# Kernel optimization log

Hardware: AMD Instinct MI355X
Metric: run time of the kernel (lower is better)

The kernel has to match this reference:

```python
import jax, jax.numpy as jnp
import numpy as np

B, TQ, TV, D = 32, 1024, 1024, 512


def setup_inputs() -> dict:
    key = jax.random.key(0)
    k1, k2, k3, k4 = jax.random.split(key, 4)
    scale = 1.0 / np.sqrt(D)
    return {
        "query": jax.random.normal(k1, (B, TQ, D), dtype=jnp.float32),
        "value": jax.random.normal(k2, (B, TV, D), dtype=jnp.float32),
        "w_weight": jax.random.normal(k3, (D, D), dtype=jnp.float32) * scale,
        "w_bias": jax.random.normal(k4, (D,), dtype=jnp.float32) * scale,
    }


def reference(query, value, w_weight, w_bias):
    # torch Linear: v @ W^T + b  -> keys [B, Tv, D]
    keys = jnp.einsum("bvd,ed->bve", value, w_weight) + w_bias
    # scores [B, Tq, Tv], softmax over Tv (last dim), unscaled as in source
    scores = jnp.einsum("bqd,bvd->bqv", query, keys)
    alignment = jax.nn.softmax(scores, axis=-1)
    context = jnp.einsum("bqv,bvd->bqd", alignment, value)
    context = jnp.concatenate([context, query], axis=-1)  # [B, Tq, 2D]
    alignment_t = jnp.swapaxes(alignment, 1, 2)  # [B, Tv, Tq]
    return context, alignment_t
```

## Files before the change

### kernel.cpp

```cpp
#include <hip/hip_runtime.h>
#include <hip/hip_bf16.h>

#define NB  32
#define NTQ 1024
#define NTV 1024
#define ND  512

typedef float f32x4 __attribute__((ext_vector_type(4)));
typedef float f32x2 __attribute__((ext_vector_type(2)));
typedef __bf16 bf16x8 __attribute__((ext_vector_type(8)));
typedef unsigned short u16x4 __attribute__((ext_vector_type(4)));
typedef unsigned short u16x8 __attribute__((ext_vector_type(8)));
typedef unsigned int u32x2 __attribute__((ext_vector_type(2)));
typedef unsigned int u32x4 __attribute__((ext_vector_type(4)));

static __device__ __forceinline__ unsigned short f2bf(float f) {
  unsigned u = __builtin_bit_cast(unsigned, f);
  u += 0x7fffu + ((u >> 16) & 1u);
  return (unsigned short)(u >> 16);
}
static __device__ __forceinline__ float bf2f(unsigned short h) {
  unsigned u = ((unsigned)h) << 16;
  return __builtin_bit_cast(float, u);
}
static __device__ __forceinline__ unsigned split2(float x) {
  unsigned u = __builtin_bit_cast(unsigned, x);
  unsigned h = u >> 16;
  float hf = __builtin_bit_cast(float, u & 0xffff0000u);
  unsigned l = __builtin_bit_cast(unsigned, x - hf) >> 16;
  return h | (l << 16);
}
static __device__ __forceinline__ f32x4 mfma16(bf16x8 a, bf16x8 b, f32x4 c) {
  return __builtin_amdgcn_mfma_f32_16x16x32_bf16(a, b, c, 0, 0, 0);
}

__global__ __launch_bounds__(256) void k_vt(const float* __restrict__ V,
                                            unsigned short* __restrict__ Vt) {
  int vt = blockIdx.x, dt = blockIdx.y, b = blockIdx.z;
  int t = threadIdx.x;
  __shared__ unsigned short L[64][72];
#pragma unroll
  for (int r = 0; r < 4; ++r) {
    int v = (t >> 4) + r * 16;
    int c4 = (t & 15) * 4;
    f32x4 x = *(const f32x4*)(V + (size_t)(b * NTV + vt * 64 + v) * ND + dt * 64 + c4);
    u16x4 h;
#pragma unroll
    for (int j = 0; j < 4; ++j) h[j] = f2bf(x[j]);
    *(u16x4*)&L[v][c4] = h;
  }
  __syncthreads();
#pragma unroll
  for (int r = 0; r < 4; ++r) {
    int d = (t >> 4) + r * 16;
    int v4 = (t & 15) * 4;
    u16x4 o;
#pragma unroll
    for (int i = 0; i < 4; ++i) o[i] = L[v4 + i][d];
    *(u16x4*)(Vt + (size_t)(b * ND + dt * 64 + d) * NTV + vt * 64 + v4) = o;
  }
}

__global__ __launch_bounds__(256, 2) void k_keys(const float* __restrict__ V,
                                                 const float* __restrict__ W,
                                                 const float* __restrict__ bias,
                                                 unsigned int* __restrict__ kbuf) {
  int bid = blockIdx.x;
  int swz = (bid & 7) * 128 + (bid >> 3);
  int bm = swz >> 2, bn = swz & 3;
  int t = threadIdx.x, lane = t & 63, w = t >> 6;
  int wr = (w >> 1) * 64, wc = (w & 1) * 64;
  __shared__ __align__(16) unsigned char SMEM[73728];
  auto Ah = (unsigned short(*)[72])(SMEM);
  auto Al = (unsigned short(*)[72])(SMEM + 18432);
  auto Bh = (unsigned short(*)[72])(SMEM + 36864);
  auto Bl = (unsigned short(*)[72])(SMEM + 55296);
  f32x4 acc[4][4] = {};
  const int row0 = bm * 128, col0 = bn * 128;
  int srow = t >> 4, c4 = (t & 15) * 4;

  f32x4 vreg[8], wreg[8];
#pragma unroll
  for (int r = 0; r < 8; ++r) {
    vreg[r] = *(const f32x4*)(V + (size_t)(row0 + srow + r * 16) * ND + c4);
    wreg[r] = *(const f32x4*)(W + (size_t)(col0 + srow + r * 16) * ND + c4);
  }
  for (int k0 = 0; k0 < ND; k0 += 64) {
    __syncthreads();
#pragma unroll
    for (int r = 0; r < 8; ++r) {
      int row = srow + r * 16;
      u16x4 h, l;
#pragma unroll
      for (int j = 0; j < 4; ++j) {
        unsigned p = split2(vreg[r][j]);
        h[j] = (unsigned short)(p & 0xffffu); l[j] = (unsigned short)(p >> 16);
      }
      *(u16x4*)&Ah[row][c4] = h; *(u16x4*)&Al[row][c4] = l;
#pragma unroll
      for (int j = 0; j < 4; ++j) {
        unsigned p = split2(wreg[r][j]);
        h[j] = (unsigned short)(p & 0xffffu); l[j] = (unsigned short)(p >> 16);
      }
      *(u16x4*)&Bh[row][c4] = h; *(u16x4*)&Bl[row][c4] = l;
    }
    __syncthreads();
    if (k0 + 64 < ND) {
#pragma unroll
      for (int r = 0; r < 8; ++r) {
        vreg[r] = *(const f32x4*)(V + (size_t)(row0 + srow + r * 16) * ND + k0 + 64 + c4);
        wreg[r] = *(const f32x4*)(W + (size_t)(col0 + srow + r * 16) * ND + k0 + 64 + c4);
      }
    }
#pragma unroll
    for (int kk = 0; kk < 2; ++kk) {
      int kof = kk * 32 + ((lane >> 4) << 3);
      bf16x8 ah[4], al[4], bh[4], bl[4];
#pragma unroll
      for (int i = 0; i < 4; ++i) {
        int ra = wr + i * 16 + (lane & 15);
        ah[i] = *(const bf16x8*)&Ah[ra][kof];
        al[i] = *(const bf16x8*)&Al[ra][kof];
        int rb = wc + i * 16 + (lane & 15);
        bh[i] = *(const bf16x8*)&Bh[rb][kof];
        bl[i] = *(const bf16x8*)&Bl[rb][kof];
      }
#pragma unroll
      for (int i = 0; i < 4; ++i)
#pragma unroll
        for (int j = 0; j < 4; ++j) {
          acc[i][j] = mfma16(ah[i], bh[j], acc[i][j]);
          acc[i][j] = mfma16(ah[i], bl[j], acc[i][j]);
          acc[i][j] = mfma16(al[i], bh[j], acc[i][j]);
        }
    }
  }
  __syncthreads();
  unsigned* CT = (unsigned*)SMEM;
#pragma unroll
  for (int j = 0; j < 4; ++j) {
    int col_l = wc + j * 16 + (lane & 15);
    float bj = bias[col0 + col_l];
#pragma unroll
    for (int i = 0; i < 4; ++i) {
      int rb_l = wr + i * 16 + ((lane >> 4) << 2);
#pragma unroll
      for (int r = 0; r < 4; ++r) CT[(rb_l + r) * 134 + col_l] = split2(acc[i][j][r] + bj);
    }
  }
  __syncthreads();
#pragma unroll
  for (int it = 0; it < 32; ++it) {
    int idx = it * 256 + t;
    int row = idx >> 6, c2 = idx & 63;
    *(u32x2*)(kbuf + (size_t)(row0 + row) * 1024 + col0 + c2 * 2) =
        *(const u32x2*)&CT[row * 134 + c2 * 2];
  }
}

__global__ __launch_bounds__(256, 2) void k_scores(const float* __restrict__ Q,
                                                   const unsigned int* __restrict__ kbuf,
                                                   unsigned short* __restrict__ ebase,
                                                   float2* __restrict__ partials) {
  int bid = blockIdx.x;
  int swz = (bid & 7) * 256 + (bid >> 3);
  int b = swz >> 6, rr2 = swz & 63, vt = rr2 >> 3, qt = rr2 & 7;
  int t = threadIdx.x, lane = t & 63, w = t >> 6, g = lane >> 4, l15 = lane & 15;
  int wr = (w >> 1) * 64, wc = (w & 1) * 64;
  __shared__ __align__(16) unsigned char SMEM[73728];
  auto Ah = (unsigned short(*)[72])(SMEM);
  auto Al = (unsigned short(*)[72])(SMEM + 18432);
  auto Bh = (unsigned short(*)[72])(SMEM + 36864);
  auto Bl = (unsigned short(*)[72])(SMEM + 55296);
  f32x4 acc[4][4] = {};
  const size_t qrow = (size_t)(b * NTQ + qt * 128);
  const size_t krow = (size_t)(b * NTV + vt * 128);
  int srow = t >> 4, c4 = (t & 15) * 4;

  f32x4 qreg[8]; u32x4 kreg[8];
#pragma unroll
  for (int r = 0; r < 8; ++r) {
    qreg[r] = *(const f32x4*)(Q + (qrow + srow + r * 16) * ND + c4);
    kreg[r] = *(const u32x4*)(kbuf + (krow + srow + r * 16) * 1024 + c4);
  }
  for (int k0 = 0; k0 < ND; k0 += 64) {
    __syncthreads();
#pragma unroll
    for (int r = 0; r < 8; ++r) {
      int row = srow + r * 16;
      u16x4 h, l;
#pragma unroll
      for (int j = 0; j < 4; ++j) {
        unsigned p = split2(qreg[r][j]);
        h[j] = (unsigned short)(p & 0xffffu); l[j] = (unsigned short)(p >> 16);
      }
      *(u16x4*)&Ah[row][c4] = h; *(u16x4*)&Al[row][c4] = l;
#pragma unroll
      for (int j = 0; j < 4; ++j) {
        h[j] = (unsigned short)(kreg[r][j] & 0xffffu);
        l[j] = (unsigned short)(kreg[r][j] >> 16);
      }
      *(u16x4*)&Bh[row][c4] = h; *(u16x4*)&Bl[row][c4] = l;
    }
    __syncthreads();
    if (k0 + 64 < ND) {
#pragma unroll
      for (int r = 0; r < 8; ++r) {
        qreg[r] = *(const f32x4*)(Q + (qrow + srow + r * 16) * ND + k0 + 64 + c4);
        kreg[r] = *(const u32x4*)(kbuf + (krow + srow + r * 16) * 1024 + k0 + 64 + c4);
      }
    }
#pragma unroll
    for (int kk = 0; kk < 2; ++kk) {
      int kof = kk * 32 + ((lane >> 4) << 3);
      bf16x8 ah[4], al[4], bh[4], bl[4];
#pragma unroll
      for (int i = 0; i < 4; ++i) {
        int ra = wr + i * 16 + (lane & 15);
        ah[i] = *(const bf16x8*)&Ah[ra][kof];
        al[i] = *(const bf16x8*)&Al[ra][kof];
        int rb = wc + i * 16 + (lane & 15);
        bh[i] = *(const bf16x8*)&Bh[rb][kof];
        bl[i] = *(const bf16x8*)&Bl[rb][kof];
      }
#pragma unroll
      for (int i = 0; i < 4; ++i)
#pragma unroll
        for (int j = 0; j < 4; ++j) {
          acc[i][j] = mfma16(ah[i], bh[j], acc[i][j]);
          acc[i][j] = mfma16(ah[i], bl[j], acc[i][j]);
          acc[i][j] = mfma16(al[i], bh[j], acc[i][j]);
        }
    }
  }
  __syncthreads();
  auto E2 = (unsigned short(*)[136])(SMEM);
  float* Lm = (float*)(SMEM + 36864);
  float* Ls = (float*)(SMEM + 37888);
#pragma unroll
  for (int i = 0; i < 4; ++i)
#pragma unroll
    for (int r = 0; r < 4; ++r) {
      float m = fmaxf(fmaxf(acc[i][0][r], acc[i][1][r]), fmaxf(acc[i][2][r], acc[i][3][r]));
#pragma unroll
      for (int msk = 1; msk < 16; msk <<= 1) m = fmaxf(m, __shfl_xor(m, msk));
      if (l15 == 0) Lm[(wr + i * 16 + g * 4 + r) * 2 + (w & 1)] = m;
    }
  __syncthreads();
#pragma unroll
  for (int i = 0; i < 4; ++i)
#pragma unroll
    for (int r = 0; r < 4; ++r) {
      int ql = wr + i * 16 + g * 4 + r;
      float mf = fmaxf(Lm[ql * 2], Lm[ql * 2 + 1]);
      float s = 0.f;
#pragma unroll
      for (int j = 0; j < 4; ++j) {
        float e = __expf(acc[i][j][r] - mf);
        s += e;
        E2[ql][wc + j * 16 + l15] = f2bf(e);
      }
#pragma unroll
      for (int msk = 1; msk < 16; msk <<= 1) s += __shfl_xor(s, msk);
      if (l15 == 0) Ls[ql * 2 + (w & 1)] = s;
    }
  __syncthreads();
  if (t < 128) {
    float mf = fmaxf(Lm[t * 2], Lm[t * 2 + 1]);
    float lf = Ls[t * 2] + Ls[t * 2 + 1];
    partials[(((size_t)(b * 8 + vt)) << 10) + qt * 128 + t] = make_float2(mf, lf);
  }
#pragma unroll
  for (int it = 0; it < 8; ++it) {
    int idx = it * 256 + t;
    int row = idx >> 4, ch = idx & 15;
    *(u16x8*)(ebase + (size_t)(b * 1024 + qt * 128 + row) * 2048 + 1024 + vt * 128 + ch * 8) =
        *(const u16x8*)&E2[row][ch * 8];
  }
}

__global__ __launch_bounds__(256) void k_combine(const float2* __restrict__ partials,
                                                 float2* __restrict__ stats) {
  int idx = blockIdx.x * 256 + threadIdx.x;
  int b = idx >> 10, q = idx & 1023;
  float2 p[8];
  float M = -3.0e38f;
#pragma unroll
  for (int vt = 0; vt < 8; ++vt) {
    p[vt] = partials[(((size_t)(b * 8 + vt)) << 10) + q];
    M = fmaxf(M, p[vt].x);
  }
  float L = 0.f;
#pragma unroll
  for (int vt = 0; vt < 8; ++vt) L += p[vt].y * __expf(p[vt].x - M);
  stats[idx] = make_float2(M, 1.0f / L);
}

__global__ __launch_bounds__(256, 3) void k_pv(const unsigned short* __restrict__ ebase,
                                               const unsigned short* __restrict__ Vt,
                                               const float2* __restrict__ stats,
                                               const float2* __restrict__ partials,
                                               float* __restrict__ out1) {
  int bid = blockIdx.x;
  int swz = (bid & 7) * 128 + (bid >> 3);
  int b = swz >> 5, qt = (swz >> 2) & 7, dt = swz & 3;
  int t = threadIdx.x, lane = t & 63, w = t >> 6;
  int l15 = lane & 15, g = lane >> 4;
  int wr = (w >> 1) * 64, wc = (w & 1) * 64;
  int q0 = qt * 128, d0 = dt * 128;
  __shared__ __align__(16) unsigned char SMEM[36864];
  auto Ae = (unsigned short(*)[72])(SMEM);
  auto Bv = (unsigned short(*)[72])(SMEM + 18432);
  f32x4 acc[4][4] = {};

  int srow = t >> 3, c8 = (t & 7) * 8;
  float M4[4], iL4[4];
#pragma unroll
  for (int k = 0; k < 4; ++k) {
    float2 st = stats[b * NTQ + q0 + srow + 32 * k];
    M4[k] = st.x; iL4[k] = st.y;
  }
  u16x8 ereg[4], vreg[4];
#pragma unroll
  for (int k = 0; k < 4; ++k) {
    ereg[k] = *(const u16x8*)(ebase + (size_t)(b * 1024 + q0 + srow + 32 * k) * 2048 + 1024 + c8);
    vreg[k] = *(const u16x8*)(Vt + ((size_t)b * ND + d0 + srow + 32 * k) * NTV + c8);
  }
  float sck[4];
  for (int v0 = 0; v0 < NTV; v0 += 64) {
    if ((v0 & 127) == 0) {
      int vt128 = v0 >> 7;
#pragma unroll
      for (int k = 0; k < 4; ++k) {
        float2 p = partials[(((size_t)(b * 8 + vt128)) << 10) + q0 + srow + 32 * k];
        sck[k] = __expf(p.x - M4[k]) * iL4[k];
      }
    }
    __syncthreads();
#pragma unroll
    for (int k = 0; k < 4; ++k) {
      int row = srow + 32 * k;
      u16x8 a;
#pragma unroll
      for (int m = 0; m < 8; ++m) a[m] = f2bf(bf2f(ereg[k][m]) * sck[k]);
      *(u16x8*)&Ae[row][c8] = a;
      *(u16x8*)&Bv[row][c8] = vreg[k];
    }
    if (v0 + 64 < NTV) {
#pragma unroll
      for (int k = 0; k < 4; ++k) {
        ereg[k] = *(const u16x8*)(ebase + (size_t)(b * 1024 + q0 + srow + 32 * k) * 2048 + 1024 + v0 + 64 + c8);
        vreg[k] = *(const u16x8*)(Vt + ((size_t)b * ND + d0 + srow + 32 * k) * NTV + v0 + 64 + c8);
      }
    }
    __syncthreads();
#pragma unroll
    for (int kk = 0; kk < 2; ++kk) {
      int kof = kk * 32 + g * 8;
      bf16x8 af[4], bfr[4];
#pragma unroll
      for (int i = 0; i < 4; ++i) af[i] = *(const bf16x8*)&Ae[wr + i * 16 + l15][kof];
#pragma unroll
      for (int j = 0; j < 4; ++j) bfr[j] = *(const bf16x8*)&Bv[wc + j * 16 + l15][kof];
#pragma unroll
      for (int i = 0; i < 4; ++i)
#pragma unroll
        for (int j = 0; j < 4; ++j) acc[i][j] = mfma16(af[i], bfr[j], acc[i][j]);
    }
  }
  float* CT = (float*)SMEM;
#pragma unroll
  for (int h = 0; h < 2; ++h) {
    __syncthreads();
    if ((w >> 1) == h) {
#pragma unroll
      for (int i = 0; i < 4; ++i)
#pragma unroll
        for (int j = 0; j < 4; ++j) {
          int ql = i * 16 + g * 4;
          int dl = wc + j * 16 + l15;
#pragma unroll
          for (int r = 0; r < 4; ++r) CT[(ql + r) * 132 + dl] = acc[i][j][r];
        }
    }
    __syncthreads();
#pragma unroll
    for (int it = 0; it < 8; ++it) {
      int idx = it * 256 + t;
      int row = idx >> 5, c4 = idx & 31;
      *(f32x4*)(out1 + (size_t)(b * NTQ + q0 + h * 64 + row) * 1024 + d0 + c4 * 4) =
          *(const f32x4*)&CT[row * 132 + c4 * 4];
    }
  }
}

__global__ __launch_bounds__(256) void k_alpha(const unsigned short* ebase,
                                               const float* __restrict__ Q,
                                               const float2* __restrict__ stats,
                                               const float2* __restrict__ partials,
                                               float* __restrict__ out2,
                                               float* out1) {
  int bid = blockIdx.x;
  int swz = (bid & 7) * 64 + (bid >> 3);
  int b = swz >> 4, qc = swz & 15;
  int q0 = qc * 64;
  int t = threadIdx.x;
  __shared__ float T[128][68];
  int row = t >> 4, ch = t & 15;
  float M4[4], iL4[4];
#pragma unroll
  for (int k = 0; k < 4; ++k) {
    float2 st = stats[b * NTQ + q0 + row + 16 * k];
    M4[k] = st.x; iL4[k] = st.y;
  }
  for (int vt = 0; vt < 8; ++vt) {
    __syncthreads();
#pragma unroll
    for (int k = 0; k < 4; ++k) {
      int r = row + 16 * k;
      float2 p = partials[(((size_t)(b * 8 + vt)) << 10) + q0 + r];
      float sc = __expf(p.x - M4[k]) * iL4[k];
      u16x8 ev = *(const u16x8*)(ebase + (size_t)(b * 1024 + q0 + r) * 2048 + 1024 + vt * 128 + ch * 8);
#pragma unroll
      for (int m = 0; m < 8; ++m) {
        int v = ch * 8 + m;
        T[v][r ^ (((v >> 3) & 7) << 3)] = bf2f(ev[m]) * sc;
      }
    }
    __syncthreads();
#pragma unroll
    for (int it = 0; it < 8; ++it) {
      int idx = it * 256 + t;
      int vr = idx >> 4, c4 = idx & 15;
      int cs = (c4 * 4) ^ (((vr >> 3) & 7) << 3);
      *(f32x4*)(out2 + ((size_t)(b * 1024) + vt * 128 + vr) * 1024 + q0 + c4 * 4) =
          *(const f32x4*)&T[vr][cs];
    }
  }
  __syncthreads();
#pragma unroll
  for (int k = 0; k < 32; ++k) {
    int idx = k * 256 + t;
    int r = idx >> 7, c4 = idx & 127;
    *(f32x4*)(out1 + (size_t)(b * 1024 + q0 + r) * 1024 + 512 + c4 * 4) =
        *(const f32x4*)(Q + (size_t)(b * 1024 + q0 + r) * 512 + c4 * 4);
  }
}

extern "C" void kernel_launch(void* const* d_in, const int* in_sizes, int n_in,
                              void* d_out, int out_size, void* d_ws, size_t ws_size,
                              hipStream_t stream) {
  const float* Q    = (const float*)d_in[0];
  const float* V    = (const float*)d_in[1];
  const float* W    = (const float*)d_in[2];
  const float* bias = (const float*)d_in[3];

  float* out1 = (float*)d_out;
  float* out2 = (float*)d_out + (size_t)NB * NTQ * (2 * ND);

  unsigned short* Vt = (unsigned short*)d_ws;
  float2* stats    = (float2*)((char*)d_ws + 33554432);
  float2* partials = (float2*)((char*)d_ws + 33554432 + 262144);

  unsigned int* kbuf = (unsigned int*)out1;
  unsigned short* ebase = (unsigned short*)out1;

  k_vt<<<dim3(16, 8, 32), 256, 0, stream>>>(V, Vt);
  k_keys<<<1024, 256, 0, stream>>>(V, W, bias, kbuf);
  k_scores<<<2048, 256, 0, stream>>>(Q, kbuf, ebase, partials);
  k_combine<<<128, 256, 0, stream>>>(partials, stats);
  k_pv<<<1024, 256, 0, stream>>>(ebase, Vt, stats, partials, out1);
  k_alpha<<<512, 256, 0, stream>>>(ebase, Q, stats, partials, out2, out1);
}
```

Baseline: 341.0 us.

## Halve K-tile and LDS footprint to raise occupancy of GEMM kernels

The keys and scores GEMM kernels now stage 32-wide K tiles instead of 64, halving shared memory per block and the number of prefetch registers. The keys epilogue writes its output through shared memory in two 64-row halves so the staging buffer still fits. Launch bounds are raised to 4 blocks per CU for keys, scores and pv, aiming to hide latency through occupancy. In exchange there are twice as many K iterations and barriers, less unrolled MFMA work per sync, and tighter register caps that risk spills.

```diff
diff --git a/kernel.cpp b/kernel.cpp
--- a/kernel.cpp
+++ b/kernel.cpp
@@ -61,7 +61,7 @@
   }
 }
 
-__global__ __launch_bounds__(256, 2) void k_keys(const float* __restrict__ V,
+__global__ __launch_bounds__(256, 4) void k_keys(const float* __restrict__ V,
                                                  const float* __restrict__ W,
                                                  const float* __restrict__ bias,
                                                  unsigned int* __restrict__ kbuf) {
@@ -69,27 +69,28 @@
   int swz = (bid & 7) * 128 + (bid >> 3);
   int bm = swz >> 2, bn = swz & 3;
   int t = threadIdx.x, lane = t & 63, w = t >> 6;
+  int l15 = lane & 15, g = lane >> 4;
   int wr = (w >> 1) * 64, wc = (w & 1) * 64;
-  __shared__ __align__(16) unsigned char SMEM[73728];
-  auto Ah = (unsigned short(*)[72])(SMEM);
-  auto Al = (unsigned short(*)[72])(SMEM + 18432);
-  auto Bh = (unsigned short(*)[72])(SMEM + 36864);
-  auto Bl = (unsigned short(*)[72])(SMEM + 55296);
+  __shared__ __align__(16) unsigned char SMEM[36864];
+  auto Ah = (unsigned short(*)[36])(SMEM);
+  auto Al = (unsigned short(*)[36])(SMEM + 9216);
+  auto Bh = (unsigned short(*)[36])(SMEM + 18432);
+  auto Bl = (unsigned short(*)[36])(SMEM + 27648);
   f32x4 acc[4][4] = {};
   const int row0 = bm * 128, col0 = bn * 128;
-  int srow = t >> 4, c4 = (t & 15) * 4;
-
-  f32x4 vreg[8], wreg[8];
-#pragma unroll
-  for (int r = 0; r < 8; ++r) {
-    vreg[r] = *(const f32x4*)(V + (size_t)(row0 + srow + r * 16) * ND + c4);
-    wreg[r] = *(const f32x4*)(W + (size_t)(col0 + srow + r * 16) * ND + c4);
-  }
-  for (int k0 = 0; k0 < ND; k0 += 64) {
-    __syncthreads();
-#pragma unroll
-    for (int r = 0; r < 8; ++r) {
-      int row = srow + r * 16;
+  int srow = t >> 3, c4 = (t & 7) * 4;
+
+  f32x4 vreg[4], wreg[4];
+#pragma unroll
+  for (int r = 0; r < 4; ++r) {
+    vreg[r] = *(const f32x4*)(V + (size_t)(row0 + srow + 32 * r) * ND + c4);
+    wreg[r] = *(const f32x4*)(W + (size_t)(col0 + srow + 32 * r) * ND + c4);
+  }
+  for (int k0 = 0; k0 < ND; k0 += 32) {
+    __syncthreads();
+#pragma unroll
+    for (int r = 0; r < 4; ++r) {
+      int row = srow + 32 * r;
       u16x4 h, l;
 #pragma unroll
       for (int j = 0; j < 4; ++j) {
@@ -105,60 +106,62 @@
       *(u16x4*)&Bh[row][c4] = h; *(u16x4*)&Bl[row][c4] = l;
     }
     __syncthreads();
-    if (k0 + 64 < ND) {
-#pragma unroll
-      for (int r = 0; r < 8; ++r) {
-        vreg[r] = *(const f32x4*)(V + (size_t)(row0 + srow + r * 16) * ND + k0 + 64 + c4);
-        wreg[r] = *(const f32x4*)(W + (size_t)(col0 + srow + r * 16) * ND + k0 + 64 + c4);
-      }
-    }
-#pragma unroll
-    for (int kk = 0; kk < 2; ++kk) {
-      int kof = kk * 32 + ((lane >> 4) << 3);
-      bf16x8 ah[4], al[4], bh[4], bl[4];
-#pragma unroll
-      for (int i = 0; i < 4; ++i) {
-        int ra = wr + i * 16 + (lane & 15);
-        ah[i] = *(const bf16x8*)&Ah[ra][kof];
-        al[i] = *(const bf16x8*)&Al[ra][kof];
-        int rb = wc + i * 16 + (lane & 15);
-        bh[i] = *(const bf16x8*)&Bh[rb][kof];
-        bl[i] = *(const bf16x8*)&Bl[rb][kof];
-      }
-#pragma unroll
-      for (int i = 0; i < 4; ++i)
-#pragma unroll
-        for (int j = 0; j < 4; ++j) {
-          acc[i][j] = mfma16(ah[i], bh[j], acc[i][j]);
-          acc[i][j] = mfma16(ah[i], bl[j], acc[i][j]);
-          acc[i][j] = mfma16(al[i], bh[j], acc[i][j]);
+    if (k0 + 32 < ND) {
+#pragma unroll
+      for (int r = 0; r < 4; ++r) {
+        vreg[r] = *(const f32x4*)(V + (size_t)(row0 + srow + 32 * r) * ND + k0 + 32 + c4);
+        wreg[r] = *(const f32x4*)(W + (size_t)(col0 + srow + 32 * r) * ND + k0 + 32 + c4);
+      }
+    }
+    int kof = g * 8;
+    bf16x8 ah[4], al[4], bh[4], bl[4];
+#pragma unroll
+    for (int i = 0; i < 4; ++i) {
+      int ra = wr + i * 16 + l15;
+      ah[i] = *(const bf16x8*)&Ah[ra][kof];
+      al[i] = *(const bf16x8*)&Al[ra][kof];
+      int rb = wc + i * 16 + l15;
+      bh[i] = *(const bf16x8*)&Bh[rb][kof];
+      bl[i] = *(const bf16x8*)&Bl[rb][kof];
+    }
+#pragma unroll
+    for (int i = 0; i < 4; ++i)
+#pragma unroll
+      for (int j = 0; j < 4; ++j) {
+        acc[i][j] = mfma16(ah[i], bh[j], acc[i][j]);
+        acc[i][j] = mfma16(ah[i], bl[j], acc[i][j]);
+        acc[i][j] = mfma16(al[i], bh[j], acc[i][j]);
+      }
+  }
+  unsigned* CT = (unsigned*)SMEM;
+#pragma unroll
+  for (int h = 0; h < 2; ++h) {
+    __syncthreads();
+    if ((w >> 1) == h) {
+#pragma unroll
+      for (int j = 0; j < 4; ++j) {
+        int col_l = wc + j * 16 + l15;
+        float bj = bias[col0 + col_l];
+#pragma unroll
+        for (int i = 0; i < 4; ++i) {
+          int rl = i * 16 + g * 4;
+#pragma unroll
+          for (int r = 0; r < 4; ++r) CT[(rl + r) * 132 + col_l] = split2(acc[i][j][r] + bj);
         }
-    }
-  }
-  __syncthreads();
-  unsigned* CT = (unsigned*)SMEM;
-#pragma unroll
-  for (int j = 0; j < 4; ++j) {
-    int col_l = wc + j * 16 + (lane & 15);
-    float bj = bias[col0 + col_l];
-#pragma unroll
-    for (int i = 0; i < 4; ++i) {
-      int rb_l = wr + i * 16 + ((lane >> 4) << 2);
-#pragma unroll
-      for (int r = 0; r < 4; ++r) CT[(rb_l + r) * 134 + col_l] = split2(acc[i][j][r] + bj);
-    }
-  }
-  __syncthreads();
-#pragma unroll
-  for (int it = 0; it < 32; ++it) {
-    int idx = it * 256 + t;
-    int row = idx >> 6, c2 = idx & 63;
-    *(u32x2*)(kbuf + (size_t)(row0 + row) * 1024 + col0 + c2 * 2) =
-        *(const u32x2*)&CT[row * 134 + c2 * 2];
-  }
-}
-
-__global__ __launch_bounds__(256, 2) void k_scores(const float* __restrict__ Q,
+      }
+    }
+    __syncthreads();
+#pragma unroll
+    for (int it = 0; it < 16; ++it) {
+      int idx = it * 256 + t;
+      int row = idx >> 6, c2 = idx & 63;
+      *(u32x2*)(kbuf + (size_t)(row0 + h * 64 + row) * 1024 + col0 + c2 * 2) =
+          *(const u32x2*)&CT[row * 132 + c2 * 2];
+    }
+  }
+}
+
+__global__ __launch_bounds__(256, 4) void k_scores(const float* __restrict__ Q,
                                                    const unsigned int* __restrict__ kbuf,
                                                    unsigned short* __restrict__ ebase,
                                                    float2* __restrict__ partials) {
@@ -167,27 +170,27 @@
   int b = swz >> 6, rr2 = swz & 63, vt = rr2 >> 3, qt = rr2 & 7;
   int t = threadIdx.x, lane = t & 63, w = t >> 6, g = lane >> 4, l15 = lane & 15;
   int wr = (w >> 1) * 64, wc = (w & 1) * 64;
-  __shared__ __align__(16) unsigned char SMEM[73728];
-  auto Ah = (unsigned short(*)[72])(SMEM);
-  auto Al = (unsigned short(*)[72])(SMEM + 18432);
-  auto Bh = (unsigned short(*)[72])(SMEM + 36864);
-  auto Bl = (unsigned short(*)[72])(SMEM + 55296);
+  __shared__ __align__(16) unsigned char SMEM[36864];
+  auto Ah = (unsigned short(*)[36])(SMEM);
+  auto Al = (unsigned short(*)[36])(SMEM + 9216);
+  auto Bh = (unsigned short(*)[36])(SMEM + 18432);
+  auto Bl = (unsigned short(*)[36])(SMEM + 27648);
   f32x4 acc[4][4] = {};
   const size_t qrow = (size_t)(b * NTQ + qt * 128);
   const size_t krow = (size_t)(b * NTV + vt * 128);
-  int srow = t >> 4, c4 = (t & 15) * 4;
-
-  f32x4 qreg[8]; u32x4 kreg[8];
-#pragma unroll
-  for (int r = 0; r < 8; ++r) {
-    qreg[r] = *(const f32x4*)(Q + (qrow + srow + r * 16) * ND + c4);
-    kreg[r] = *(const u32x4*)(kbuf + (krow + srow + r * 16) * 1024 + c4);
-  }
-  for (int k0 = 0; k0 < ND; k0 += 64) {
-    __syncthreads();
-#pragma unroll
-    for (int r = 0; r < 8; ++r) {
-      int row = srow + r * 16;
+  int srow = t >> 3, c4 = (t & 7) * 4;
+
+  f32x4 qreg[4]; u32x4 kreg[4];
+#pragma unroll
+  for (int r = 0; r < 4; ++r) {
+    qreg[r] = *(const f32x4*)(Q + (qrow + srow + 32 * r) * ND + c4);
+    kreg[r] = *(const u32x4*)(kbuf + (krow + srow + 32 * r) * 1024 + c4);
+  }
+  for (int k0 = 0; k0 < ND; k0 += 32) {
+    __syncthreads();
+#pragma unroll
+    for (int r = 0; r < 4; ++r) {
+      int row = srow + 32 * r;
       u16x4 h, l;
 #pragma unroll
       for (int j = 0; j < 4; ++j) {
@@ -203,40 +206,37 @@
       *(u16x4*)&Bh[row][c4] = h; *(u16x4*)&Bl[row][c4] = l;
     }
     __syncthreads();
-    if (k0 + 64 < ND) {
-#pragma unroll
-      for (int r = 0; r < 8; ++r) {
-        qreg[r] = *(const f32x4*)(Q + (qrow + srow + r * 16) * ND + k0 + 64 + c4);
-        kreg[r] = *(const u32x4*)(kbuf + (krow + srow + r * 16) * 1024 + k0 + 64 + c4);
-      }
-    }
-#pragma unroll
-    for (int kk = 0; kk < 2; ++kk) {
-      int kof = kk * 32 + ((lane >> 4) << 3);
-      bf16x8 ah[4], al[4], bh[4], bl[4];
-#pragma unroll
-      for (int i = 0; i < 4; ++i) {
-        int ra = wr + i * 16 + (lane & 15);
-        ah[i] = *(const bf16x8*)&Ah[ra][kof];
-        al[i] = *(const bf16x8*)&Al[ra][kof];
-        int rb = wc + i * 16 + (lane & 15);
-        bh[i] = *(const bf16x8*)&Bh[rb][kof];
-        bl[i] = *(const bf16x8*)&Bl[rb][kof];
-      }
-#pragma unroll
-      for (int i = 0; i < 4; ++i)
-#pragma unroll
-        for (int j = 0; j < 4; ++j) {
-          acc[i][j] = mfma16(ah[i], bh[j], acc[i][j]);
-          acc[i][j] = mfma16(ah[i], bl[j], acc[i][j]);
-          acc[i][j] = mfma16(al[i], bh[j], acc[i][j]);
-        }
-    }
+    if (k0 + 32 < ND) {
+#pragma unroll
+      for (int r = 0; r < 4; ++r) {
+        qreg[r] = *(const f32x4*)(Q + (qrow + srow + 32 * r) * ND + k0 + 32 + c4);
+        kreg[r] = *(const u32x4*)(kbuf + (krow + srow + 32 * r) * 1024 + k0 + 32 + c4);
+      }
+    }
+    int kof = g * 8;
+    bf16x8 ah[4], al[4], bh[4], bl[4];
+#pragma unroll
+    for (int i = 0; i < 4; ++i) {
+      int ra = wr + i * 16 + l15;
+      ah[i] = *(const bf16x8*)&Ah[ra][kof];
+      al[i] = *(const bf16x8*)&Al[ra][kof];
+      int rb = wc + i * 16 + l15;
+      bh[i] = *(const bf16x8*)&Bh[rb][kof];
+      bl[i] = *(const bf16x8*)&Bl[rb][kof];
+    }
+#pragma unroll
+    for (int i = 0; i < 4; ++i)
+#pragma unroll
+      for (int j = 0; j < 4; ++j) {
+        acc[i][j] = mfma16(ah[i], bh[j], acc[i][j]);
+        acc[i][j] = mfma16(ah[i], bl[j], acc[i][j]);
+        acc[i][j] = mfma16(al[i], bh[j], acc[i][j]);
+      }
   }
   __syncthreads();
   auto E2 = (unsigned short(*)[136])(SMEM);
-  float* Lm = (float*)(SMEM + 36864);
-  float* Ls = (float*)(SMEM + 37888);
+  float* Lm = (float*)(SMEM + 34816);
+  float* Ls = (float*)(SMEM + 35840);
 #pragma unroll
   for (int i = 0; i < 4; ++i)
 #pragma unroll
@@ -296,7 +296,7 @@
   stats[idx] = make_float2(M, 1.0f / L);
 }
 
-__global__ __launch_bounds__(256, 3) void k_pv(const unsigned short* __restrict__ ebase,
+__global__ __launch_bounds__(256, 4) void k_pv(const unsigned short* __restrict__ ebase,
                                                const unsigned short* __restrict__ Vt,
                                                const float2* __restrict__ stats,
                                                const float2* __restrict__ partials,
```

After: 796.8 us. 2.34x slower.

## Pre-split Q into bf16 hi/lo planes and stream scores operands via global-to-LDS loads

Applied to the files above, without the earlier changes.

Adds a kernel that splits Q into separate bf16 high and low planes ahead of time. k_keys now writes keys as separate hi/lo planes instead of packed words. k_scores loads both operands directly into LDS with global_load_lds using an XOR-swizzled layout, which removes the per-tile register staging and split work and shrinks LDS use. The costs are an extra pass over Q, the scratch buffer placed in out2, and giving up the register prefetch overlap, since the occupancy hint of 2 blocks was dropped from launch bounds.

```diff
diff --git a/kernel.cpp b/kernel.cpp
--- a/kernel.cpp
+++ b/kernel.cpp
@@ -33,6 +33,10 @@
 static __device__ __forceinline__ f32x4 mfma16(bf16x8 a, bf16x8 b, f32x4 c) {
   return __builtin_amdgcn_mfma_f32_16x16x32_bf16(a, b, c, 0, 0, 0);
 }
+static __device__ __forceinline__ void gload16(const unsigned short* g, unsigned short* l) {
+  __builtin_amdgcn_global_load_lds((const __attribute__((address_space(1))) unsigned*)g,
+                                   (__attribute__((address_space(3))) unsigned*)l, 16, 0, 0);
+}
 
 __global__ __launch_bounds__(256) void k_vt(const float* __restrict__ V,
                                             unsigned short* __restrict__ Vt) {
@@ -61,14 +65,36 @@
   }
 }
 
+__global__ __launch_bounds__(256) void k_qsplit(const float* __restrict__ Q,
+                                                unsigned short* __restrict__ qsp) {
+  int base = blockIdx.x * 1024 + threadIdx.x;
+#pragma unroll
+  for (int k = 0; k < 4; ++k) {
+    int idx = base + k * 256;
+    int row = idx >> 7;
+    int e4 = (idx & 127) * 4;
+    f32x4 x = *(const f32x4*)(Q + (size_t)row * 512 + e4);
+    u16x4 hi, lo;
+#pragma unroll
+    for (int j = 0; j < 4; ++j) {
+      unsigned p = split2(x[j]);
+      hi[j] = (unsigned short)(p & 0xffffu);
+      lo[j] = (unsigned short)(p >> 16);
+    }
+    *(u16x4*)(qsp + (size_t)row * 1024 + e4) = hi;
+    *(u16x4*)(qsp + (size_t)row * 1024 + 512 + e4) = lo;
+  }
+}
+
 __global__ __launch_bounds__(256, 2) void k_keys(const float* __restrict__ V,
                                                  const float* __restrict__ W,
                                                  const float* __restrict__ bias,
-                                                 unsigned int* __restrict__ kbuf) {
+                                                 unsigned short* __restrict__ kp) {
   int bid = blockIdx.x;
   int swz = (bid & 7) * 128 + (bid >> 3);
   int bm = swz >> 2, bn = swz & 3;
   int t = threadIdx.x, lane = t & 63, w = t >> 6;
+  int l15 = lane & 15, g = lane >> 4;
   int wr = (w >> 1) * 64, wc = (w & 1) * 64;
   __shared__ __align__(16) unsigned char SMEM[73728];
   auto Ah = (unsigned short(*)[72])(SMEM);
@@ -114,14 +140,14 @@
     }
 #pragma unroll
     for (int kk = 0; kk < 2; ++kk) {
-      int kof = kk * 32 + ((lane >> 4) << 3);
+      int kof = kk * 32 + g * 8;
       bf16x8 ah[4], al[4], bh[4], bl[4];
 #pragma unroll
       for (int i = 0; i < 4; ++i) {
-        int ra = wr + i * 16 + (lane & 15);
+        int ra = wr + i * 16 + l15;
         ah[i] = *(const bf16x8*)&Ah[ra][kof];
         al[i] = *(const bf16x8*)&Al[ra][kof];
-        int rb = wc + i * 16 + (lane & 15);
+        int rb = wc + i * 16 + l15;
         bh[i] = *(const bf16x8*)&Bh[rb][kof];
         bl[i] = *(const bf16x8*)&Bl[rb][kof];
       }
@@ -139,89 +165,79 @@
   unsigned* CT = (unsigned*)SMEM;
 #pragma unroll
   for (int j = 0; j < 4; ++j) {
-    int col_l = wc + j * 16 + (lane & 15);
+    int col_l = wc + j * 16 + l15;
     float bj = bias[col0 + col_l];
 #pragma unroll
     for (int i = 0; i < 4; ++i) {
-      int rb_l = wr + i * 16 + ((lane >> 4) << 2);
-#pragma unroll
-      for (int r = 0; r < 4; ++r) CT[(rb_l + r) * 134 + col_l] = split2(acc[i][j][r] + bj);
-    }
-  }
-  __syncthreads();
-#pragma unroll
-  for (int it = 0; it < 32; ++it) {
+      int rb_l = wr + i * 16 + g * 4;
+#pragma unroll
+      for (int r = 0; r < 4; ++r) CT[(rb_l + r) * 136 + col_l] = split2(acc[i][j][r] + bj);
+    }
+  }
+  __syncthreads();
+#pragma unroll
+  for (int it = 0; it < 16; ++it) {
     int idx = it * 256 + t;
-    int row = idx >> 6, c2 = idx & 63;
-    *(u32x2*)(kbuf + (size_t)(row0 + row) * 1024 + col0 + c2 * 2) =
-        *(const u32x2*)&CT[row * 134 + c2 * 2];
-  }
-}
-
-__global__ __launch_bounds__(256, 2) void k_scores(const float* __restrict__ Q,
-                                                   const unsigned int* __restrict__ kbuf,
-                                                   unsigned short* __restrict__ ebase,
-                                                   float2* __restrict__ partials) {
+    int row = idx >> 5, cc = (idx & 31) * 4;
+    u32x4 p = *(const u32x4*)&CT[row * 136 + cc];
+    u16x4 hi, lo;
+#pragma unroll
+    for (int j = 0; j < 4; ++j) {
+      hi[j] = (unsigned short)(p[j] & 0xffffu);
+      lo[j] = (unsigned short)(p[j] >> 16);
+    }
+    size_t rbase = (size_t)(row0 + row) * 2048 + col0;
+    *(u16x4*)(kp + rbase + cc) = hi;
+    *(u16x4*)(kp + rbase + 512 + cc) = lo;
+  }
+}
+
+__global__ __launch_bounds__(256) void k_scores(const unsigned short* __restrict__ qsp,
+                                                const unsigned short* kp,
+                                                unsigned short* ebase,
+                                                float2* __restrict__ partials) {
   int bid = blockIdx.x;
   int swz = (bid & 7) * 256 + (bid >> 3);
   int b = swz >> 6, rr2 = swz & 63, vt = rr2 >> 3, qt = rr2 & 7;
   int t = threadIdx.x, lane = t & 63, w = t >> 6, g = lane >> 4, l15 = lane & 15;
   int wr = (w >> 1) * 64, wc = (w & 1) * 64;
-  __shared__ __align__(16) unsigned char SMEM[73728];
-  auto Ah = (unsigned short(*)[72])(SMEM);
-  auto Al = (unsigned short(*)[72])(SMEM + 18432);
-  auto Bh = (unsigned short(*)[72])(SMEM + 36864);
-  auto Bl = (unsigned short(*)[72])(SMEM + 55296);
+  __shared__ __align__(16) unsigned char SMEM[65536];
+  unsigned short* lds = (unsigned short*)SMEM;
   f32x4 acc[4][4] = {};
   const size_t qrow = (size_t)(b * NTQ + qt * 128);
   const size_t krow = (size_t)(b * NTV + vt * 128);
-  int srow = t >> 4, c4 = (t & 15) * 4;
-
-  f32x4 qreg[8]; u32x4 kreg[8];
-#pragma unroll
-  for (int r = 0; r < 8; ++r) {
-    qreg[r] = *(const f32x4*)(Q + (qrow + srow + r * 16) * ND + c4);
-    kreg[r] = *(const u32x4*)(kbuf + (krow + srow + r * 16) * 1024 + c4);
-  }
+  int grow = lane >> 3;
+  int gcg = lane & 7;
+
   for (int k0 = 0; k0 < ND; k0 += 64) {
     __syncthreads();
 #pragma unroll
-    for (int r = 0; r < 8; ++r) {
-      int row = srow + r * 16;
-      u16x4 h, l;
-#pragma unroll
-      for (int j = 0; j < 4; ++j) {
-        unsigned p = split2(qreg[r][j]);
-        h[j] = (unsigned short)(p & 0xffffu); l[j] = (unsigned short)(p >> 16);
-      }
-      *(u16x4*)&Ah[row][c4] = h; *(u16x4*)&Al[row][c4] = l;
-#pragma unroll
-      for (int j = 0; j < 4; ++j) {
-        h[j] = (unsigned short)(kreg[r][j] & 0xffffu);
-        l[j] = (unsigned short)(kreg[r][j] >> 16);
-      }
-      *(u16x4*)&Bh[row][c4] = h; *(u16x4*)&Bl[row][c4] = l;
-    }
-    __syncthreads();
-    if (k0 + 64 < ND) {
-#pragma unroll
-      for (int r = 0; r < 8; ++r) {
-        qreg[r] = *(const f32x4*)(Q + (qrow + srow + r * 16) * ND + k0 + 64 + c4);
-        kreg[r] = *(const u32x4*)(kbuf + (krow + srow + r * 16) * 1024 + k0 + 64 + c4);
-      }
-    }
+    for (int i = 0; i < 4; ++i) {
+      int c = i * 4 + w;
+      int row = c * 8 + grow;
+      int scg = gcg ^ (row & 7);
+      const unsigned short* ga = qsp + (qrow + row) * 1024 + k0 + scg * 8;
+      const unsigned short* gb = kp + (krow + row) * 2048 + k0 + scg * 8;
+      unsigned short* lb = lds + c * 512;
+      gload16(ga,        lb);
+      gload16(ga + 512,  lb + 8192);
+      gload16(gb,        lb + 16384);
+      gload16(gb + 512,  lb + 24576);
+    }
+    __syncthreads();
 #pragma unroll
     for (int kk = 0; kk < 2; ++kk) {
-      int kof = kk * 32 + ((lane >> 4) << 3);
       bf16x8 ah[4], al[4], bh[4], bl[4];
 #pragma unroll
       for (int i = 0; i < 4; ++i) {
-        int ra = wr + i * 16 + (lane & 15);
-        ah[i] = *(const bf16x8*)&Ah[ra][kof];
-        al[i] = *(const bf16x8*)&Al[ra][kof];
-        int rb = wc + i * 16 + (lane & 15);
-        bh[i] = *(const bf16x8*)&Bh[rb][kof];
-        bl[i] = *(const bf16x8*)&Bl[rb][kof];
+        int ra = wr + i * 16 + l15;
+        int go = ((kk * 4 + g) ^ (ra & 7)) * 8;
+        ah[i] = *(const bf16x8*)(lds + ra * 64 + go);
+        al[i] = *(const bf16x8*)(lds + 8192 + ra * 64 + go);
+        int rb = wc + i * 16 + l15;
+        int go2 = ((kk * 4 + g) ^ (rb & 7)) * 8;
+        bh[i] = *(const bf16x8*)(lds + 16384 + rb * 64 + go2);
+        bl[i] = *(const bf16x8*)(lds + 24576 + rb * 64 + go2);
       }
 #pragma unroll
       for (int i = 0; i < 4; ++i)
@@ -235,8 +251,8 @@
   }
   __syncthreads();
   auto E2 = (unsigned short(*)[136])(SMEM);
-  float* Lm = (float*)(SMEM + 36864);
-  float* Ls = (float*)(SMEM + 37888);
+  float* Lm = (float*)(SMEM + 34816);
+  float* Ls = (float*)(SMEM + 35840);
 #pragma unroll
   for (int i = 0; i < 4; ++i)
 #pragma unroll
@@ -398,7 +414,7 @@
                                                const float* __restrict__ Q,
                                                const float2* __restrict__ stats,
                                                const float2* __restrict__ partials,
-                                               float* __restrict__ out2,
+                                               float* out2,
                                                float* out1) {
   int bid = blockIdx.x;
   int swz = (bid & 7) * 64 + (bid >> 3);
@@ -462,12 +478,14 @@
   float2* stats    = (float2*)((char*)d_ws + 33554432);
   float2* partials = (float2*)((char*)d_ws + 33554432 + 262144);
 
-  unsigned int* kbuf = (unsigned int*)out1;
+  unsigned short* kp = (unsigned short*)out1;
   unsigned short* ebase = (unsigned short*)out1;
+  unsigned short* qsp = (unsigned short*)out2;
 
   k_vt<<<dim3(16, 8, 32), 256, 0, stream>>>(V, Vt);
-  k_keys<<<1024, 256, 0, stream>>>(V, W, bias, kbuf);
-  k_scores<<<2048, 256, 0, stream>>>(Q, kbuf, ebase, partials);
+  k_qsplit<<<4096, 256, 0, stream>>>(Q, qsp);
+  k_keys<<<1024, 256, 0, stream>>>(V, W, bias, kp);
+  k_scores<<<2048, 256, 0, stream>>>(qsp, kp, ebase, partials);
   k_combine<<<128, 256, 0, stream>>>(partials, stats);
   k_pv<<<1024, 256, 0, stream>>>(ebase, Vt, stats, partials, out1);
   k_alpha<<<512, 256, 0, stream>>>(ebase, Q, stats, partials, out2, out1);
```

New measurement: 369.0 us. 8.2% more time.
